# Performance work log

Hardware: AMD Instinct MI355X
Metric: run time of the kernel (lower is better)

Reference implementation:

```python
import jax, jax.numpy as jnp
import numpy as np

MARGIN = 2.0


def setup_inputs() -> dict:
    key = jax.random.key(0)
    k1, k2 = jax.random.split(key)
    predict = jax.random.normal(k1, (8192, 2048, 1, 1), dtype=jnp.float32)
    gt = jax.random.randint(k2, (8192, 1), 0, 751, dtype=jnp.int64)
    return {"predict": predict, "gt": gt}


def reference(predict, gt):
    # predict: [B, 2048, 1, 1] -> [B, D]
    p = predict.reshape(predict.shape[0], -1)
    b, d = p.shape
    # pairwise squared L2 distance / dim, via GEMM (||a||^2 + ||b||^2 - 2 a.b)
    sq = jnp.sum(p * p, axis=1)  # [B]
    d2 = (sq[:, None] + sq[None, :] - 2.0 * (p @ p.T))
    d2 = jnp.maximum(d2, 0.0) / d  # clamp tiny negatives from GEMM roundoff
    g = gt.reshape(-1)
    label = (g[:, None] == g[None, :]).astype(p.dtype)  # [B, B]
    term = label * d2 + (1.0 - label) * jax.nn.relu(MARGIN - d2)
    # original loop sums over j >= i (diagonal contributes 0: same label, dist 0)
    mask = jnp.triu(jnp.ones((b, b), dtype=bool))
    loss = jnp.sum(jnp.where(mask, term, 0.0))
    return 2.0 * loss / (b * (b - 1))
```

## Files before the change

### kernel.cpp

```cpp
#include <hip/hip_runtime.h>
#include <stdint.h>

#define NROWS 8192
#define DIM   2048
#define MARGIN 2.0f
#define SCALEQ (127.0f / 6.0f)
#define S2     ((6.0f / 127.0f) * (6.0f / 127.0f))

#define BT2     256
#define BKB     128
#define NKT     (DIM / BKB)
#define NT2     (NROWS / BT2)
#define NTILES2 (NT2 * (NT2 + 1) / 2)
#define NQ      16
#define ABUF_B  32768
#define BUF_B   65536
#define HALF_B  16384

typedef __attribute__((ext_vector_type(4)))  int  int4v;
typedef __attribute__((ext_vector_type(16))) int  int16v;
typedef unsigned char uchar;

__device__ __forceinline__ void decode_tile(int bid, int* ti, int* tj) {
    float fn = (float)NT2 + 0.5f;
    int r = (int)(fn - sqrtf(fn * fn - 2.0f * (float)bid));
    if (r < 0) r = 0;
    if (r >= NT2) r = NT2 - 1;
    while ((r + 1) * NT2 - ((r + 1) * r) / 2 <= bid) ++r;
    while (r * NT2 - (r * (r - 1)) / 2 > bid) --r;
    *ti = r;
    *tj = r + (bid - (r * NT2 - (r * (r - 1)) / 2));
}

__device__ __forceinline__ uint pack4(float4 v) {
    int q0 = (int)__builtin_rintf(v.x * SCALEQ);
    int q1 = (int)__builtin_rintf(v.y * SCALEQ);
    int q2 = (int)__builtin_rintf(v.z * SCALEQ);
    int q3 = (int)__builtin_rintf(v.w * SCALEQ);
    q0 = min(max(q0, -127), 127); q1 = min(max(q1, -127), 127);
    q2 = min(max(q2, -127), 127); q3 = min(max(q3, -127), 127);
    return (uint)(q0 & 0xFF) | ((uint)(q1 & 0xFF) << 8) |
           ((uint)(q2 & 0xFF) << 16) | ((uint)(q3 & 0xFF) << 24);
}

__global__ __launch_bounds__(256) void prep_kernel(const float* __restrict__ p,
                                                   uchar* __restrict__ pb,
                                                   float* __restrict__ sq) {
    int row = blockIdx.x;
    int t = threadIdx.x;
    const float4* prow = (const float4*)(p + (size_t)row * DIM);
    uint* qrow = (uint*)(pb + (size_t)row * DIM);
    float4 a = prow[t];
    float4 b = prow[t + 256];
    float s = a.x * a.x + a.y * a.y + a.z * a.z + a.w * a.w
            + b.x * b.x + b.y * b.y + b.z * b.z + b.w * b.w;
    qrow[t] = pack4(a);
    qrow[t + 256] = pack4(b);
#pragma unroll
    for (int o = 32; o > 0; o >>= 1) s += __shfl_down(s, o, 64);
    __shared__ float wsums[4];
    int lane = t & 63, wvv = t >> 6;
    if (lane == 0) wsums[wvv] = s;
    __syncthreads();
    if (t == 0) sq[row] = wsums[0] + wsums[1] + wsums[2] + wsums[3];
}

__device__ __forceinline__ void stage_ht(const uchar* __restrict__ pb,
                                         uchar* lds, int t, int which,
                                         int ibase, int jbase, int tid) {
    if (t >= NKT) t -= 2;
    const int h = which & 1;
    const int row0 = ((which >= 2) ? jbase : ibase) + h * 128;
    const uchar* g0 = pb + (size_t)row0 * DIM + t * BKB;
    uchar* l0 = lds + (t & 1) * BUF_B + ((which >= 2) ? ABUF_B : 0) + h * HALF_B;
#pragma unroll
    for (int r = 0; r < 2; ++r) {
        int row = r * 64 + (tid >> 3);
        int c8 = (tid & 7) ^ ((tid >> 3) & 7);
        const uchar* g = g0 + (size_t)row * DIM + c8 * 16;
        uchar* l = l0 + r * 8192 + (tid >> 6) * 1024;
        __builtin_amdgcn_global_load_lds(
            (const __attribute__((address_space(1))) uint32_t*)g,
            (__attribute__((address_space(3))) uint32_t*)l, 16, 0, 0);
    }
}

__device__ __forceinline__ void stage_qA(const uchar* __restrict__ pb,
                                         uchar* lds, int t, int ibase, int tid) {
    if (t >= NKT) t -= 2;
    const uchar* g0 = pb + (size_t)ibase * DIM + t * BKB;
    uchar* l0 = lds + (t & 1) * BUF_B;
    int row = tid >> 3;
    int c8 = (tid & 7) ^ ((tid >> 3) & 7);
    const uchar* g = g0 + (size_t)row * DIM + c8 * 16;
    uchar* l = l0 + (tid >> 6) * 1024;
    __builtin_amdgcn_global_load_lds(
        (const __attribute__((address_space(1))) uint32_t*)g,
        (__attribute__((address_space(3))) uint32_t*)l, 16, 0, 0);
}

#define BARF()   do { __builtin_amdgcn_s_barrier(); \
                      asm volatile("" ::: "memory"); } while (0)
#define WLG4()   asm volatile("s_waitcnt lgkmcnt(4)" ::: "memory")
#define WLG0()   asm volatile("s_waitcnt lgkmcnt(0)" ::: "memory")
#define WAITV8() asm volatile("s_waitcnt vmcnt(8)" ::: "memory")
#define WAITV5() asm volatile("s_waitcnt vmcnt(5)" ::: "memory")
#define WAITV0() asm volatile("s_waitcnt vmcnt(0)" ::: "memory")
#define PRIO1()  __builtin_amdgcn_s_setprio(1)
#define PRIO0()  __builtin_amdgcn_s_setprio(0)
#define SB0()    __builtin_amdgcn_sched_barrier(0)

#define RD_A(DST, MH)                                                          \
    _Pragma("unroll") for (int mt = 0; mt < 2; ++mt)                           \
    _Pragma("unroll") for (int s = 0; s < 4; ++s) {                            \
        int rl = wr * 128 + ((MH) * 2 + mt) * 32 + (lane & 31);                \
        DST[mt][s] = *(const int4v*)&Ab[rl * 128 +                             \
                      (((2 * s + kh) ^ (lane & 7)) * 16)];                     \
    }

#define RD_B(DST, NH)                                                          \
    _Pragma("unroll") for (int s = 0; s < 4; ++s) {                            \
        int rl = wc * 64 + (NH) * 32 + (lane & 31);                            \
        DST[s] = *(const int4v*)&Bb[rl * 128 +                                 \
                  (((2 * s + kh) ^ (lane & 7)) * 16)];                         \
    }

#define MFMA_QR(AF, BF, MH, NH, S0, S1)                                        \
    _Pragma("unroll") for (int s = (S0); s < (S1); ++s)                        \
    _Pragma("unroll") for (int mt = 0; mt < 2; ++mt)                           \
        acc[(MH) * 2 + mt][NH] = __builtin_amdgcn_mfma_i32_32x32x32_i8(        \
            AF[mt][s], BF[s], acc[(MH) * 2 + mt][NH], 0, 0, 0);

#define STEP_FULL(T, BUF)                                                      \
    {                                                                          \
        const uchar* Ab = &lds[(BUF) * BUF_B];                                 \
        const uchar* Bb = &lds[(BUF) * BUF_B + ABUF_B];                        \
        RD_A(af0, 0); RD_B(bf0, 0);                                            \
        SB0();                                                                 \
        RD_B(bf1, 1);                                                          \
        WLG4(); SB0();                                                         \
        PRIO1(); MFMA_QR(af0, bf0, 0, 0, 0, 4); PRIO0();                       \
        WLG0(); SB0();                                                         \
        PRIO1(); MFMA_QR(af0, bf1, 0, 1, 0, 2); PRIO0();                       \
        SB0();                                                                 \
        RD_A(af1, 1);                                                          \
        PRIO1(); MFMA_QR(af0, bf1, 0, 1, 2, 4); PRIO0();                       \
        BARF();                                                                \
        stage_ht(pb, lds, (T) + 2, 2, ibase, jbase, tid);                      \
        stage_ht(pb, lds, (T) + 2, 3, ibase, jbase, tid);                      \
        WLG0(); SB0();                                                         \
        PRIO1(); MFMA_QR(af1, bf0, 1, 0, 0, 4); PRIO0();                       \
        BARF();                                                                \
        stage_ht(pb, lds, (T) + 2, 0, ibase, jbase, tid);                      \
        stage_ht(pb, lds, (T) + 2, 1, ibase, jbase, tid);                      \
        PRIO1(); MFMA_QR(af1, bf1, 1, 1, 0, 4); PRIO0();                       \
        WAITV8(); BARF();                                                      \
    }

#define STEP_Q(T, BUF)                                                         \
    {                                                                          \
        const uchar* Ab = &lds[(BUF) * BUF_B];                                 \
        const uchar* Bb = &lds[(BUF) * BUF_B + ABUF_B];                        \
        _Pragma("unroll") for (int mt = 0; mt < 2; ++mt)                       \
        _Pragma("unroll") for (int s = 0; s < 4; ++s) {                        \
            int rl = mt * 32 + (lane & 31);                                    \
            aq[mt][s] = *(const int4v*)&Ab[rl * 128 +                          \
                         (((2 * s + kh) ^ (lane & 7)) * 16)];                  \
        }                                                                      \
        _Pragma("unroll") for (int s = 0; s < 4; ++s) {                        \
            int rl = wv * 32 + (lane & 31);                                    \
            bq[s] = *(const int4v*)&Bb[rl * 128 +                              \
                     (((2 * s + kh) ^ (lane & 7)) * 16)];                      \
        }                                                                      \
        WLG0(); SB0();                                                         \
        PRIO1();                                                               \
        _Pragma("unroll") for (int s = 0; s < 4; ++s)                          \
        _Pragma("unroll") for (int mt = 0; mt < 2; ++mt)                       \
            accq[mt] = __builtin_amdgcn_mfma_i32_32x32x32_i8(                  \
                aq[mt][s], bq[s], accq[mt], 0, 0, 0);                          \
        PRIO0();                                                               \
        BARF();                                                                \
        stage_qA(pb, lds, (T) + 2, ibase, tid);                                \
        stage_ht(pb, lds, (T) + 2, 2, ibase, jbase, tid);                      \
        stage_ht(pb, lds, (T) + 2, 3, ibase, jbase, tid);                      \
        WAITV5(); BARF();                                                      \
    }

__global__ __launch_bounds__(512) void tile2_kernel(
    const uchar* __restrict__ pb, const float* __restrict__ sq,
    const int* __restrict__ gt, double* __restrict__ accum) {

    __shared__ uchar lds[2 * BUF_B];
    __shared__ float wsum[8];

    const int bx = (int)blockIdx.x;
    const bool is_q = (bx < 4 * NQ);
    int bid, qq = 0;
    if (is_q) { bid = bx >> 2; qq = bx & 3; }
    else { int f = bx - 4 * NQ; bid = NQ + ((f & 7) << 6) + (f >> 3); }

    int ti, tj;
    decode_tile(bid, &ti, &tj);

    const int tid = threadIdx.x;
    const int lane = tid & 63;
    const int kh = lane >> 5;
    const int wv = tid >> 6;
    const int wr = wv >> 2;
    const int wc = wv & 3;
    const int jbase = tj * BT2;
    const int ibase = ti * BT2 + (is_q ? qq * 64 : 0);

    const float invd = 1.0f / (float)DIM;
    float lsum = 0.f;

    if (!is_q) {
        int16v acc[4][2] = {};
        int4v af0[2][4], af1[2][4];
        int4v bf0[4], bf1[4];

        stage_ht(pb, lds, 0, 2, ibase, jbase, tid);
        stage_ht(pb, lds, 0, 3, ibase, jbase, tid);
        stage_ht(pb, lds, 0, 0, ibase, jbase, tid);
        stage_ht(pb, lds, 0, 1, ibase, jbase, tid);
        stage_ht(pb, lds, 1, 2, ibase, jbase, tid);
        stage_ht(pb, lds, 1, 3, ibase, jbase, tid);
        stage_ht(pb, lds, 1, 0, ibase, jbase, tid);
        stage_ht(pb, lds, 1, 1, ibase, jbase, tid);
        WAITV8();
        BARF();

#pragma unroll 1
        for (int s0 = 0; s0 < NKT; s0 += 2) {
            STEP_FULL(s0, 0);
            STEP_FULL(s0 + 1, 1);
        }
        WAITV0();
        BARF();

        int j0 = jbase + wc * 64 + (lane & 31);
        float sqj[2]; int gj[2];
#pragma unroll
        for (int n = 0; n < 2; ++n) { int j = j0 + n * 32; sqj[n] = sq[j]; gj[n] = gt[j]; }
        const float wb = (ti != tj) ? 2.0f : 1.0f;
#pragma unroll
        for (int mi = 0; mi < 4; ++mi) {
#pragma unroll
            for (int q = 0; q < 4; ++q) {
#pragma unroll
                for (int rr = 0; rr < 4; ++rr) {
                    int i = ibase + wr * 128 + mi * 32 + rr + 8 * q + 4 * kh;
                    float sqi = sq[i];
                    int gi = gt[i];
#pragma unroll
                    for (int n = 0; n < 2; ++n) {
                        int j = j0 + n * 32;
                        float dot = S2 * (float)acc[mi][n][q * 4 + rr];
                        float d2 = fmaxf(sqi + sqj[n] - 2.0f * dot, 0.0f) * invd;
                        float term = (gi == gj[n]) ? d2 : fmaxf(MARGIN - d2, 0.0f);
                        float w = wb;
                        if (ti == tj && i == j) w = 2.0f;
                        lsum += w * term;
                    }
                }
            }
        }
    } else {
        int16v accq[2] = {};
        int4v aq[2][4], bq[4];

        stage_qA(pb, lds, 0, ibase, tid);
        stage_ht(pb, lds, 0, 2, ibase, jbase, tid);
        stage_ht(pb, lds, 0, 3, ibase, jbase, tid);
        stage_qA(pb, lds, 1, ibase, tid);
        stage_ht(pb, lds, 1, 2, ibase, jbase, tid);
        stage_ht(pb, lds, 1, 3, ibase, jbase, tid);
        WAITV5();
        BARF();

#pragma unroll 1
        for (int s0 = 0; s0 < NKT; s0 += 2) {
            STEP_Q(s0, 0);
            STEP_Q(s0 + 1, 1);
        }
        WAITV0();
        BARF();

        int j = jbase + wv * 32 + (lane & 31);
        float sqj = sq[j];
        int gj = gt[j];
        const float wb = (ti != tj) ? 2.0f : 1.0f;
#pragma unroll
        for (int mt = 0; mt < 2; ++mt) {
#pragma unroll
            for (int q = 0; q < 4; ++q) {
#pragma unroll
                for (int rr = 0; rr < 4; ++rr) {
                    int i = ibase + mt * 32 + rr + 8 * q + 4 * kh;
                    float dot = S2 * (float)accq[mt][q * 4 + rr];
                    float d2 = fmaxf(sq[i] + sqj - 2.0f * dot, 0.0f) * invd;
                    float term = (gt[i] == gj) ? d2 : fmaxf(MARGIN - d2, 0.0f);
                    float w = wb;
                    if (ti == tj && i == j) w = 2.0f;
                    lsum += w * term;
                }
            }
        }
    }

#pragma unroll
    for (int o = 32; o > 0; o >>= 1) lsum += __shfl_down(lsum, o, 64);
    if (lane == 0) wsum[wv] = lsum;
    __syncthreads();
    if (tid == 0) {
        float s = 0.f;
#pragma unroll
        for (int w = 0; w < 8; ++w) s += wsum[w];
        atomicAdd(accum, (double)s);
    }
}

__global__ void finalize_kernel(const double* __restrict__ accum,
                                float* __restrict__ out) {
    if (threadIdx.x == 0)
        out[0] = (float)(accum[0] * (1.0 / ((double)NROWS * (double)(NROWS - 1))));
}

extern "C" void kernel_launch(void* const* d_in, const int* in_sizes, int n_in,
                              void* d_out, int out_size, void* d_ws, size_t ws_size,
                              hipStream_t stream) {
    (void)in_sizes; (void)n_in; (void)out_size; (void)ws_size;
    const float* p = (const float*)d_in[0];
    const int* gt = (const int*)d_in[1];
    float* out = (float*)d_out;

    uchar* pb = (uchar*)d_ws;
    size_t off = (size_t)NROWS * DIM;
    float* sq = (float*)((char*)d_ws + off);
    off += (size_t)NROWS * sizeof(float);
    double* accum = (double*)((char*)d_ws + off);

    (void)hipMemsetAsync(accum, 0, sizeof(double), stream);
    prep_kernel<<<NROWS, 256, 0, stream>>>(p, pb, sq);
    tile2_kernel<<<4 * NQ + 512, 512, 0, stream>>>(pb, sq, gt, accum);
    finalize_kernel<<<1, 64, 0, stream>>>(accum, out);
}
```

Measured before the change: 112.7 us.

## Fully unroll the int8 GEMM K-loop and restructure LDS layout and read schedule

Moves the A and B regions of LDS into separate contiguous halves, precomputes per-lane swizzled LDS offsets, and fully unrolls the 16-step K loop with compile-time staging addresses. The main-tile step now uses a single A-fragment register set and inserts extra barriers with full lgkm waits between LDS reads and each MFMA quarter, replacing the earlier partial-wait overlap. The aim is fewer address computations and lower register pressure, at the cost of more barriers and less overlap between LDS reads and MFMAs, plus larger code size.

```diff
diff --git a/kernel.cpp b/kernel.cpp
--- a/kernel.cpp
+++ b/kernel.cpp
@@ -13,9 +13,7 @@
 #define NT2     (NROWS / BT2)
 #define NTILES2 (NT2 * (NT2 + 1) / 2)
 #define NQ      16
-#define ABUF_B  32768
-#define BUF_B   65536
-#define HALF_B  16384
+#define BREG    65536
 
 typedef __attribute__((ext_vector_type(4)))  int  int4v;
 typedef __attribute__((ext_vector_type(16))) int  int16v;
@@ -65,14 +63,16 @@
     if (t == 0) sq[row] = wsums[0] + wsums[1] + wsums[2] + wsums[3];
 }
 
-__device__ __forceinline__ void stage_ht(const uchar* __restrict__ pb,
-                                         uchar* lds, int t, int which,
-                                         int ibase, int jbase, int tid) {
-    if (t >= NKT) t -= 2;
-    const int h = which & 1;
-    const int row0 = ((which >= 2) ? jbase : ibase) + h * 128;
+template<int TT, int WHICH>
+__device__ __forceinline__ void stage_c(const uchar* __restrict__ pb, uchar* lds,
+                                        int ibase, int jbase, int tid) {
+    constexpr int t   = (TT >= NKT) ? TT - 2 : TT;
+    constexpr int buf = t & 1;
+    constexpr int h   = WHICH & 1;
+    constexpr bool isB = (WHICH >= 2);
+    const int row0 = (isB ? jbase : ibase) + h * 128;
     const uchar* g0 = pb + (size_t)row0 * DIM + t * BKB;
-    uchar* l0 = lds + (t & 1) * BUF_B + ((which >= 2) ? ABUF_B : 0) + h * HALF_B;
+    uchar* l0 = lds + (isB ? BREG : 0) + buf * 32768 + h * 16384;
 #pragma unroll
     for (int r = 0; r < 2; ++r) {
         int row = r * 64 + (tid >> 3);
@@ -85,11 +85,27 @@
     }
 }
 
-__device__ __forceinline__ void stage_qA(const uchar* __restrict__ pb,
-                                         uchar* lds, int t, int ibase, int tid) {
+__device__ __forceinline__ void stage_qB(const uchar* __restrict__ pb, uchar* lds,
+                                         int t, int h, int jbase, int tid) {
+    if (t >= NKT) t -= 2;
+    const uchar* g0 = pb + (size_t)(jbase + h * 128) * DIM + t * BKB;
+    uchar* l0 = lds + BREG + (t & 1) * 32768 + h * 16384;
+#pragma unroll
+    for (int r = 0; r < 2; ++r) {
+        int row = r * 64 + (tid >> 3);
+        int c8 = (tid & 7) ^ ((tid >> 3) & 7);
+        const uchar* g = g0 + (size_t)row * DIM + c8 * 16;
+        uchar* l = l0 + r * 8192 + (tid >> 6) * 1024;
+        __builtin_amdgcn_global_load_lds(
+            (const __attribute__((address_space(1))) uint32_t*)g,
+            (__attribute__((address_space(3))) uint32_t*)l, 16, 0, 0);
+    }
+}
+__device__ __forceinline__ void stage_qA(const uchar* __restrict__ pb, uchar* lds,
+                                         int t, int ibase, int tid) {
     if (t >= NKT) t -= 2;
     const uchar* g0 = pb + (size_t)ibase * DIM + t * BKB;
-    uchar* l0 = lds + (t & 1) * BUF_B;
+    uchar* l0 = lds + (t & 1) * 32768;
     int row = tid >> 3;
     int c8 = (tid & 7) ^ ((tid >> 3) & 7);
     const uchar* g = g0 + (size_t)row * DIM + c8 * 16;
@@ -101,8 +117,7 @@
 
 #define BARF()   do { __builtin_amdgcn_s_barrier(); \
                       asm volatile("" ::: "memory"); } while (0)
-#define WLG4()   asm volatile("s_waitcnt lgkmcnt(4)" ::: "memory")
-#define WLG0()   asm volatile("s_waitcnt lgkmcnt(0)" ::: "memory")
+#define WAITL()  asm volatile("s_waitcnt lgkmcnt(0)" ::: "memory")
 #define WAITV8() asm volatile("s_waitcnt vmcnt(8)" ::: "memory")
 #define WAITV5() asm volatile("s_waitcnt vmcnt(5)" ::: "memory")
 #define WAITV0() asm volatile("s_waitcnt vmcnt(0)" ::: "memory")
@@ -110,69 +125,55 @@
 #define PRIO0()  __builtin_amdgcn_s_setprio(0)
 #define SB0()    __builtin_amdgcn_sched_barrier(0)
 
-#define RD_A(DST, MH)                                                          \
+#define RD_A_C(MH, BUFO)                                                       \
     _Pragma("unroll") for (int mt = 0; mt < 2; ++mt)                           \
-    _Pragma("unroll") for (int s = 0; s < 4; ++s) {                            \
-        int rl = wr * 128 + ((MH) * 2 + mt) * 32 + (lane & 31);                \
-        DST[mt][s] = *(const int4v*)&Ab[rl * 128 +                             \
-                      (((2 * s + kh) ^ (lane & 7)) * 16)];                     \
-    }
-
-#define RD_B(DST, NH)                                                          \
-    _Pragma("unroll") for (int s = 0; s < 4; ++s) {                            \
-        int rl = wc * 64 + (NH) * 32 + (lane & 31);                            \
-        DST[s] = *(const int4v*)&Bb[rl * 128 +                                 \
-                  (((2 * s + kh) ^ (lane & 7)) * 16)];                         \
-    }
-
-#define MFMA_QR(AF, BF, MH, NH, S0, S1)                                        \
-    _Pragma("unroll") for (int s = (S0); s < (S1); ++s)                        \
+    _Pragma("unroll") for (int s = 0; s < 4; ++s)                              \
+        af[mt][s] = *(const int4v*)&lds[acomb[s] +                             \
+                     (((MH) * 2 + mt) * 4096 + (BUFO))];
+
+#define RD_B_C(DST, NH, BUFO)                                                  \
+    _Pragma("unroll") for (int s = 0; s < 4; ++s)                              \
+        DST[s] = *(const int4v*)&lds[bcomb[s] + ((NH) * 4096 + (BUFO))];
+
+#define MFMAQ(MH, BF, NH)                                                      \
     _Pragma("unroll") for (int mt = 0; mt < 2; ++mt)                           \
+    _Pragma("unroll") for (int s = 0; s < 4; ++s)                              \
         acc[(MH) * 2 + mt][NH] = __builtin_amdgcn_mfma_i32_32x32x32_i8(        \
-            AF[mt][s], BF[s], acc[(MH) * 2 + mt][NH], 0, 0, 0);
-
-#define STEP_FULL(T, BUF)                                                      \
+            af[mt][s], BF[s], acc[(MH) * 2 + mt][NH], 0, 0, 0);
+
+#define STEPF(T)                                                               \
     {                                                                          \
-        const uchar* Ab = &lds[(BUF) * BUF_B];                                 \
-        const uchar* Bb = &lds[(BUF) * BUF_B + ABUF_B];                        \
-        RD_A(af0, 0); RD_B(bf0, 0);                                            \
-        SB0();                                                                 \
-        RD_B(bf1, 1);                                                          \
-        WLG4(); SB0();                                                         \
-        PRIO1(); MFMA_QR(af0, bf0, 0, 0, 0, 4); PRIO0();                       \
-        WLG0(); SB0();                                                         \
-        PRIO1(); MFMA_QR(af0, bf1, 0, 1, 0, 2); PRIO0();                       \
-        SB0();                                                                 \
-        RD_A(af1, 1);                                                          \
-        PRIO1(); MFMA_QR(af0, bf1, 0, 1, 2, 4); PRIO0();                       \
+        constexpr int BUFO = ((T) & 1) * 32768;                                \
+        RD_A_C(0, BUFO);                                                       \
+        RD_B_C(bf0, 0, BUFO);                                                  \
+        BARF(); WAITL(); SB0();                                                \
+        PRIO1(); MFMAQ(0, bf0, 0); PRIO0();                                    \
         BARF();                                                                \
-        stage_ht(pb, lds, (T) + 2, 2, ibase, jbase, tid);                      \
-        stage_ht(pb, lds, (T) + 2, 3, ibase, jbase, tid);                      \
-        WLG0(); SB0();                                                         \
-        PRIO1(); MFMA_QR(af1, bf0, 1, 0, 0, 4); PRIO0();                       \
+        RD_B_C(bf1, 1, BUFO);                                                  \
+        BARF(); WAITL(); SB0();                                                \
+        PRIO1(); MFMAQ(0, bf1, 1); PRIO0();                                    \
         BARF();                                                                \
-        stage_ht(pb, lds, (T) + 2, 0, ibase, jbase, tid);                      \
-        stage_ht(pb, lds, (T) + 2, 1, ibase, jbase, tid);                      \
-        PRIO1(); MFMA_QR(af1, bf1, 1, 1, 0, 4); PRIO0();                       \
+        RD_A_C(1, BUFO);                                                       \
+        stage_c<(T) + 2, 2>(pb, lds, ibase, jbase, tid);                       \
+        stage_c<(T) + 2, 3>(pb, lds, ibase, jbase, tid);                       \
+        BARF(); WAITL(); SB0();                                                \
+        PRIO1(); MFMAQ(1, bf0, 0); PRIO0();                                    \
+        BARF();                                                                \
+        stage_c<(T) + 2, 0>(pb, lds, ibase, jbase, tid);                       \
+        stage_c<(T) + 2, 1>(pb, lds, ibase, jbase, tid);                       \
+        PRIO1(); MFMAQ(1, bf1, 1); PRIO0();                                    \
         WAITV8(); BARF();                                                      \
     }
 
-#define STEP_Q(T, BUF)                                                         \
+#define STEP_Q(T)                                                              \
     {                                                                          \
-        const uchar* Ab = &lds[(BUF) * BUF_B];                                 \
-        const uchar* Bb = &lds[(BUF) * BUF_B + ABUF_B];                        \
+        const int qb = ((T) & 1) * 32768;                                      \
         _Pragma("unroll") for (int mt = 0; mt < 2; ++mt)                       \
-        _Pragma("unroll") for (int s = 0; s < 4; ++s) {                        \
-            int rl = mt * 32 + (lane & 31);                                    \
-            aq[mt][s] = *(const int4v*)&Ab[rl * 128 +                          \
-                         (((2 * s + kh) ^ (lane & 7)) * 16)];                  \
-        }                                                                      \
-        _Pragma("unroll") for (int s = 0; s < 4; ++s) {                        \
-            int rl = wv * 32 + (lane & 31);                                    \
-            bq[s] = *(const int4v*)&Bb[rl * 128 +                              \
-                     (((2 * s + kh) ^ (lane & 7)) * 16)];                      \
-        }                                                                      \
-        WLG0(); SB0();                                                         \
+        _Pragma("unroll") for (int s = 0; s < 4; ++s)                          \
+            aq[mt][s] = *(const int4v*)&lds[aqc[s] + mt * 4096 + qb];          \
+        _Pragma("unroll") for (int s = 0; s < 4; ++s)                          \
+            bq[s] = *(const int4v*)&lds[bqc[s] + qb];                          \
+        WAITL(); SB0();                                                        \
         PRIO1();                                                               \
         _Pragma("unroll") for (int s = 0; s < 4; ++s)                          \
         _Pragma("unroll") for (int mt = 0; mt < 2; ++mt)                       \
@@ -181,8 +182,8 @@
         PRIO0();                                                               \
         BARF();                                                                \
         stage_qA(pb, lds, (T) + 2, ibase, tid);                                \
-        stage_ht(pb, lds, (T) + 2, 2, ibase, jbase, tid);                      \
-        stage_ht(pb, lds, (T) + 2, 3, ibase, jbase, tid);                      \
+        stage_qB(pb, lds, (T) + 2, 0, jbase, tid);                             \
+        stage_qB(pb, lds, (T) + 2, 1, jbase, tid);                             \
         WAITV5(); BARF();                                                      \
     }
 
@@ -190,7 +191,7 @@
     const uchar* __restrict__ pb, const float* __restrict__ sq,
     const int* __restrict__ gt, double* __restrict__ accum) {
 
-    __shared__ uchar lds[2 * BUF_B];
+    __shared__ uchar lds[131072];
     __shared__ float wsum[8];
 
     const int bx = (int)blockIdx.x;
@@ -216,25 +217,33 @@
 
     if (!is_q) {
         int16v acc[4][2] = {};
-        int4v af0[2][4], af1[2][4];
+        int4v af[2][4];
         int4v bf0[4], bf1[4];
 
-        stage_ht(pb, lds, 0, 2, ibase, jbase, tid);
-        stage_ht(pb, lds, 0, 3, ibase, jbase, tid);
-        stage_ht(pb, lds, 0, 0, ibase, jbase, tid);
-        stage_ht(pb, lds, 0, 1, ibase, jbase, tid);
-        stage_ht(pb, lds, 1, 2, ibase, jbase, tid);
-        stage_ht(pb, lds, 1, 3, ibase, jbase, tid);
-        stage_ht(pb, lds, 1, 0, ibase, jbase, tid);
-        stage_ht(pb, lds, 1, 1, ibase, jbase, tid);
+        int acomb[4], bcomb[4];
+#pragma unroll
+        for (int s = 0; s < 4; ++s) {
+            int slot = ((2 * s + kh) ^ (lane & 7)) * 16;
+            acomb[s] = (wr * 128 + (lane & 31)) * 128 + slot;
+            bcomb[s] = BREG + (wc * 64 + (lane & 31)) * 128 + slot;
+        }
+
+        stage_c<0, 2>(pb, lds, ibase, jbase, tid);
+        stage_c<0, 3>(pb, lds, ibase, jbase, tid);
+        stage_c<0, 0>(pb, lds, ibase, jbase, tid);
+        stage_c<0, 1>(pb, lds, ibase, jbase, tid);
+        stage_c<1, 2>(pb, lds, ibase, jbase, tid);
+        stage_c<1, 3>(pb, lds, ibase, jbase, tid);
+        stage_c<1, 0>(pb, lds, ibase, jbase, tid);
+        stage_c<1, 1>(pb, lds, ibase, jbase, tid);
         WAITV8();
         BARF();
 
-#pragma unroll 1
-        for (int s0 = 0; s0 < NKT; s0 += 2) {
-            STEP_FULL(s0, 0);
-            STEP_FULL(s0 + 1, 1);
-        }
+        STEPF(0);  STEPF(1);  STEPF(2);  STEPF(3);
+        STEPF(4);  STEPF(5);  STEPF(6);  STEPF(7);
+        STEPF(8);  STEPF(9);  STEPF(10); STEPF(11);
+        STEPF(12); STEPF(13); STEPF(14); STEPF(15);
+
         WAITV0();
         BARF();
 
@@ -269,19 +278,27 @@
         int16v accq[2] = {};
         int4v aq[2][4], bq[4];
 
+        int aqc[4], bqc[4];
+#pragma unroll
+        for (int s = 0; s < 4; ++s) {
+            int slot = ((2 * s + kh) ^ (lane & 7)) * 16;
+            aqc[s] = (lane & 31) * 128 + slot;
+            bqc[s] = BREG + (wv * 32 + (lane & 31)) * 128 + slot;
+        }
+
         stage_qA(pb, lds, 0, ibase, tid);
-        stage_ht(pb, lds, 0, 2, ibase, jbase, tid);
-        stage_ht(pb, lds, 0, 3, ibase, jbase, tid);
+        stage_qB(pb, lds, 0, 0, jbase, tid);
+        stage_qB(pb, lds, 0, 1, jbase, tid);
         stage_qA(pb, lds, 1, ibase, tid);
-        stage_ht(pb, lds, 1, 2, ibase, jbase, tid);
-        stage_ht(pb, lds, 1, 3, ibase, jbase, tid);
+        stage_qB(pb, lds, 1, 0, jbase, tid);
+        stage_qB(pb, lds, 1, 1, jbase, tid);
         WAITV5();
         BARF();
 
 #pragma unroll 1
         for (int s0 = 0; s0 < NKT; s0 += 2) {
-            STEP_Q(s0, 0);
-            STEP_Q(s0 + 1, 1);
+            STEP_Q(s0);
+            STEP_Q(s0 + 1);
         }
         WAITV0();
         BARF();
```

Result: slower. 116.2 us (+3.1%).
